# Kernel optimization log

Hardware: AMD Instinct MI355X
Metric: run time of the kernel (lower is better)

Reference implementation:

```python
import jax, jax.numpy as jnp
import numpy as np


def setup_inputs() -> dict:
    key = jax.random.key(0)
    k1, k2 = jax.random.split(key)
    N, C, D, Hg, Wg = 2, 12, 8, 16, 16
    H, W = 1024, 1024
    grid = jax.random.normal(k1, (N, C, D, Hg, Wg), dtype=jnp.float32)
    guidemap = jax.random.uniform(k2, (N, 1, H, W), dtype=jnp.float32)
    return {"grid": grid, "guidemap": guidemap}


def reference(grid, guidemap):
    # Bilateral grid slicing: 3D trilinear grid_sample, padding='border', align_corners=True.
    # grid: [N, C, D, Hg, Wg]; guidemap: [N, 1, H, W] -> out: [N, C, H, W]
    N, C, D, Hg, Wg = grid.shape
    _, _, H, W = guidemap.shape

    # Normalized sample coords in [-1, 1] (meshgrid over output pixels).
    yn = jnp.linspace(-1.0, 1.0, H)                      # [H]
    xn = jnp.linspace(-1.0, 1.0, W)                      # [W]
    zn = guidemap[:, 0] * 2.0 - 1.0                      # [N, H, W]

    # Unnormalize (align_corners=True) and clamp to border.
    iy = jnp.clip((yn + 1.0) * 0.5 * (Hg - 1), 0.0, Hg - 1.0)  # [H]
    ix = jnp.clip((xn + 1.0) * 0.5 * (Wg - 1), 0.0, Wg - 1.0)  # [W]
    iz = jnp.clip((zn + 1.0) * 0.5 * (D - 1), 0.0, D - 1.0)    # [N, H, W]

    iy0 = jnp.floor(iy).astype(jnp.int32)
    ix0 = jnp.floor(ix).astype(jnp.int32)
    iy1 = jnp.minimum(iy0 + 1, Hg - 1)
    ix1 = jnp.minimum(ix0 + 1, Wg - 1)
    wy = (iy - iy0)[:, None]                              # [H, 1]
    wx = (ix - ix0)[None, :]                              # [1, W]

    Y0, Y1 = iy0[:, None], iy1[:, None]                   # [H, 1]
    X0, X1 = ix0[None, :], ix1[None, :]                   # [1, W]

    iz0 = jnp.floor(iz).astype(jnp.int32)                 # [N, H, W]
    iz1 = jnp.minimum(iz0 + 1, D - 1)
    wz = iz - iz0                                         # [N, H, W]

    def sample_one(g, z0, z1, wzn):
        # g: [C, D, Hg, Wg]; z0, z1, wzn: [H, W]
        def gat(zz, yy, xx):
            return g[:, zz, yy, xx]                       # [C, H, W]
        # interpolate along z first, then x, then y
        c00 = gat(z0, Y0, X0) * (1.0 - wzn) + gat(z1, Y0, X0) * wzn
        c01 = gat(z0, Y0, X1) * (1.0 - wzn) + gat(z1, Y0, X1) * wzn
        c10 = gat(z0, Y1, X0) * (1.0 - wzn) + gat(z1, Y1, X0) * wzn
        c11 = gat(z0, Y1, X1) * (1.0 - wzn) + gat(z1, Y1, X1) * wzn
        c0 = c00 * (1.0 - wx) + c01 * wx
        c1 = c10 * (1.0 - wx) + c11 * wx
        return c0 * (1.0 - wy) + c1 * wy                  # [C, H, W]

    coeff = jax.vmap(sample_one)(grid, iz0, iz1, wz)      # [N, C, H, W]
    return coeff
```

## Files before the change

### kernel.cpp

```cpp
#include <hip/hip_runtime.h>

#define H 1024
#define W 1024
#define NC 12
#define ND 8
#define HG 16
#define WG 16

__global__ __launch_bounds__(256) void slice_kernel(
    const float* __restrict__ grid,
    const float* __restrict__ guide,
    float* __restrict__ out)
{
    const int y   = blockIdx.x;
    const int n   = blockIdx.y;
    const int tid = threadIdx.x;

    float yn = -1.0f + 2.0f * (float)y / (float)(H - 1);
    float iy = (yn + 1.0f) * 0.5f * (float)(HG - 1);
    iy = fminf(fmaxf(iy, 0.0f), (float)(HG - 1));
    int   iy0 = (int)floorf(iy);
    int   iy1 = min(iy0 + 1, HG - 1);
    float wy  = iy - (float)iy0;

    __shared__ __align__(16) float sg[WG * ND * NC];
    const float* gbase = grid + (size_t)n * NC * ND * HG * WG;
    for (int i = tid; i < WG * ND * NC; i += 256) {
        int x  = i & (WG - 1);
        int zc = i >> 4;
        int z  = zc & (ND - 1);
        int c  = zc >> 3;
        const float* gp = gbase + ((c * ND + z) * HG) * WG + x;
        float r0 = gp[iy0 * WG];
        float r1 = gp[iy1 * WG];
        sg[(x * ND + z) * NC + c] = r0 + (r1 - r0) * wy;
    }
    __syncthreads();

    const int xb = tid * 4;
    const float* gd = guide + ((size_t)n * H + y) * W;
    float*       ob = out + ((size_t)n * NC * H + y) * W;

    const float4 g4 = *(const float4*)&gd[xb];
    const float gz[4] = {g4.x, g4.y, g4.z, g4.w};

    float res[NC][4];

    #pragma unroll
    for (int p = 0; p < 4; ++p) {
        const int x = xb + p;
        float xn = -1.0f + 2.0f * (float)x / (float)(W - 1);
        float ix = (xn + 1.0f) * 0.5f * (float)(WG - 1);
        ix = fminf(fmaxf(ix, 0.0f), (float)(WG - 1));
        int   ix0 = (int)floorf(ix);
        int   ix1 = min(ix0 + 1, WG - 1);
        float wx  = ix - (float)ix0;

        float zn = gz[p] * 2.0f - 1.0f;
        float iz = (zn + 1.0f) * 0.5f * (float)(ND - 1);
        iz = fminf(fmaxf(iz, 0.0f), (float)(ND - 1));
        int   iz0 = (int)floorf(iz);
        int   iz1 = min(iz0 + 1, ND - 1);
        float wz  = iz - (float)iz0;

        const int B0 = ix0 * (ND * NC);
        const int B1 = ix1 * (ND * NC);
        const int Z0 = iz0 * NC;
        const int Z1 = iz1 * NC;

        #pragma unroll
        for (int cc = 0; cc < NC; cc += 4) {
            const float4 a0 = *(const float4*)&sg[B0 + Z0 + cc];
            const float4 a1 = *(const float4*)&sg[B0 + Z1 + cc];
            const float4 b0 = *(const float4*)&sg[B1 + Z0 + cc];
            const float4 b1 = *(const float4*)&sg[B1 + Z1 + cc];

            float za, zb;
            za = a0.x + (a1.x - a0.x) * wz;
            zb = b0.x + (b1.x - b0.x) * wz;
            res[cc + 0][p] = za + (zb - za) * wx;

            za = a0.y + (a1.y - a0.y) * wz;
            zb = b0.y + (b1.y - b0.y) * wz;
            res[cc + 1][p] = za + (zb - za) * wx;

            za = a0.z + (a1.z - a0.z) * wz;
            zb = b0.z + (b1.z - b0.z) * wz;
            res[cc + 2][p] = za + (zb - za) * wx;

            za = a0.w + (a1.w - a0.w) * wz;
            zb = b0.w + (b1.w - b0.w) * wz;
            res[cc + 3][p] = za + (zb - za) * wx;
        }
    }

    #pragma unroll
    for (int c = 0; c < NC; ++c) {
        float4 v = make_float4(res[c][0], res[c][1], res[c][2], res[c][3]);
        *(float4*)&ob[(size_t)c * H * W + xb] = v;
    }
}

extern "C" void kernel_launch(void* const* d_in, const int* in_sizes, int n_in,
                              void* d_out, int out_size, void* d_ws, size_t ws_size,
                              hipStream_t stream) {
    const float* grid  = (const float*)d_in[0];
    const float* guide = (const float*)d_in[1];
    float* out = (float*)d_out;

    dim3 grd(H, 2);
    dim3 blk(256);
    slice_kernel<<<grd, blk, 0, stream>>>(grid, guide, out);
}
```

Baseline: 122.0 us.

## Split rows across two blocks, use nontemporal float2 stores, interleave channel stores

Each row is now handled by two blocks of 256 threads with 2 pixels per thread instead of 4, which doubles the grid size and lowers per-thread register pressure, with a launch-bounds occupancy hint added. Output is written per channel group right after it is computed, using nontemporal float2 stores instead of buffering all 12 channels and then issuing float4 stores. The aim is better occupancy and less cache pollution on a write-bound kernel. In exchange, each block redoes the shared grid preload, so that work is duplicated, and the stores are narrower.

```diff
diff --git a/kernel.cpp b/kernel.cpp
--- a/kernel.cpp
+++ b/kernel.cpp
@@ -7,13 +7,16 @@
 #define HG 16
 #define WG 16
 
-__global__ __launch_bounds__(256) void slice_kernel(
+typedef float v2f __attribute__((ext_vector_type(2)));
+
+__global__ __launch_bounds__(256, 6) void slice_kernel(
     const float* __restrict__ grid,
     const float* __restrict__ guide,
     float* __restrict__ out)
 {
-    const int y   = blockIdx.x;
-    const int n   = blockIdx.y;
+    const int xh  = blockIdx.x;
+    const int y   = blockIdx.y;
+    const int n   = blockIdx.z;
     const int tid = threadIdx.x;
 
     float yn = -1.0f + 2.0f * (float)y / (float)(H - 1);
@@ -37,67 +40,72 @@
     }
     __syncthreads();
 
-    const int xb = tid * 4;
+    const int xb = xh * (W / 2) + tid * 2;
     const float* gd = guide + ((size_t)n * H + y) * W;
     float*       ob = out + ((size_t)n * NC * H + y) * W;
 
-    const float4 g4 = *(const float4*)&gd[xb];
-    const float gz[4] = {g4.x, g4.y, g4.z, g4.w};
+    const float2 g2 = *(const float2*)&gd[xb];
+    const float gz[2] = {g2.x, g2.y};
 
-    float res[NC][4];
+    int   B0[2], B1[2], Z0[2], Z1[2];
+    float wxv[2], wzv[2];
 
     #pragma unroll
-    for (int p = 0; p < 4; ++p) {
+    for (int p = 0; p < 2; ++p) {
         const int x = xb + p;
         float xn = -1.0f + 2.0f * (float)x / (float)(W - 1);
         float ix = (xn + 1.0f) * 0.5f * (float)(WG - 1);
         ix = fminf(fmaxf(ix, 0.0f), (float)(WG - 1));
         int   ix0 = (int)floorf(ix);
         int   ix1 = min(ix0 + 1, WG - 1);
-        float wx  = ix - (float)ix0;
+        wxv[p] = ix - (float)ix0;
 
         float zn = gz[p] * 2.0f - 1.0f;
         float iz = (zn + 1.0f) * 0.5f * (float)(ND - 1);
         iz = fminf(fmaxf(iz, 0.0f), (float)(ND - 1));
         int   iz0 = (int)floorf(iz);
         int   iz1 = min(iz0 + 1, ND - 1);
-        float wz  = iz - (float)iz0;
+        wzv[p] = iz - (float)iz0;
 
-        const int B0 = ix0 * (ND * NC);
-        const int B1 = ix1 * (ND * NC);
-        const int Z0 = iz0 * NC;
-        const int Z1 = iz1 * NC;
+        B0[p] = ix0 * (ND * NC);
+        B1[p] = ix1 * (ND * NC);
+        Z0[p] = iz0 * NC;
+        Z1[p] = iz1 * NC;
+    }
 
+    #pragma unroll
+    for (int cc = 0; cc < NC; cc += 4) {
+        float r[2][4];
         #pragma unroll
-        for (int cc = 0; cc < NC; cc += 4) {
-            const float4 a0 = *(const float4*)&sg[B0 + Z0 + cc];
-            const float4 a1 = *(const float4*)&sg[B0 + Z1 + cc];
-            const float4 b0 = *(const float4*)&sg[B1 + Z0 + cc];
-            const float4 b1 = *(const float4*)&sg[B1 + Z1 + cc];
+        for (int p = 0; p < 2; ++p) {
+            const float wz = wzv[p], wx = wxv[p];
+            const float4 a0 = *(const float4*)&sg[B0[p] + Z0[p] + cc];
+            const float4 a1 = *(const float4*)&sg[B0[p] + Z1[p] + cc];
+            const float4 b0 = *(const float4*)&sg[B1[p] + Z0[p] + cc];
+            const float4 b1 = *(const float4*)&sg[B1[p] + Z1[p] + cc];
 
             float za, zb;
             za = a0.x + (a1.x - a0.x) * wz;
             zb = b0.x + (b1.x - b0.x) * wz;
-            res[cc + 0][p] = za + (zb - za) * wx;
+            r[p][0] = za + (zb - za) * wx;
 
             za = a0.y + (a1.y - a0.y) * wz;
             zb = b0.y + (b1.y - b0.y) * wz;
-            res[cc + 1][p] = za + (zb - za) * wx;
+            r[p][1] = za + (zb - za) * wx;
 
             za = a0.z + (a1.z - a0.z) * wz;
             zb = b0.z + (b1.z - b0.z) * wz;
-            res[cc + 2][p] = za + (zb - za) * wx;
+            r[p][2] = za + (zb - za) * wx;
 
             za = a0.w + (a1.w - a0.w) * wz;
             zb = b0.w + (b1.w - b0.w) * wz;
-            res[cc + 3][p] = za + (zb - za) * wx;
+            r[p][3] = za + (zb - za) * wx;
         }
-    }
-
-    #pragma unroll
-    for (int c = 0; c < NC; ++c) {
-        float4 v = make_float4(res[c][0], res[c][1], res[c][2], res[c][3]);
-        *(float4*)&ob[(size_t)c * H * W + xb] = v;
+        #pragma unroll
+        for (int c = 0; c < 4; ++c) {
+            v2f v = {r[0][c], r[1][c]};
+            __builtin_nontemporal_store(v, (v2f*)&ob[(size_t)(cc + c) * H * W + xb]);
+        }
     }
 }
 
@@ -108,7 +116,7 @@
     const float* guide = (const float*)d_in[1];
     float* out = (float*)d_out;
 
-    dim3 grd(H, 2);
+    dim3 grd(2, H, 2);
     dim3 blk(256);
     slice_kernel<<<grd, blk, 0, stream>>>(grid, guide, out);
 }
```

Result: slower. 128.3 us (+5.1%).
